# Optimization experiments

Measured on AMD Instinct MI355X. Metric: run time of the kernel, lower is better.

The kernel has to match this reference:

```python
import jax, jax.numpy as jnp
import numpy as np

B, S, D, H = 4, 1024, 1024, 16
HD = D // H  # head dim = 64


def setup_inputs() -> dict:
    key = jax.random.key(0)
    ks = jax.random.split(key, 12)
    inv = 1.0 / np.sqrt(D)
    inp = {
        "q": jax.random.normal(ks[0], (B, S, D), jnp.float32),
        "k": jax.random.normal(ks[1], (B, S, D), jnp.float32),
        "v": jax.random.normal(ks[2], (B, S, D), jnp.float32),
        # additive-style mask: 1 where attention is disallowed (causal)
        "mask": jnp.triu(jnp.ones((S, S), jnp.float32), k=1)[None, None, :, :],
        "Wq": jax.random.normal(ks[3], (D, D), jnp.float32) * inv,
        "bq": jnp.zeros((D,), jnp.float32),
        "Wk": jax.random.normal(ks[4], (D, D), jnp.float32) * inv,
        "bk": jnp.zeros((D,), jnp.float32),
        "Wv": jax.random.normal(ks[5], (D, D), jnp.float32) * inv,
        "bv": jnp.zeros((D,), jnp.float32),
        "Wo": jax.random.normal(ks[6], (D, D), jnp.float32) * inv,
        "bo": jnp.zeros((D,), jnp.float32),
    }
    return inp


def _split_heads(x):
    # [b, s, (h d)] -> [b, h, s, d]
    b, s, _ = x.shape
    return x.reshape(b, s, H, HD).transpose(0, 2, 1, 3)


def reference(q, k, v, mask, Wq, bq, Wk, bk, Wv, bv, Wo, bo):
    query = _split_heads(q @ Wq + bq)   # [b,h,s,d]
    key = _split_heads(k @ Wk + bk)
    value = _split_heads(v @ Wv + bv)

    scores = jnp.einsum("bhqd,bhkd->bhqk", query, key) / np.sqrt(HD)
    scores = scores + mask * (-1e12)
    attention_weights = jax.nn.softmax(scores, axis=-1)  # [b,h,s,s]
    attn = jnp.einsum("bhqk,bhkd->bhqd", attention_weights, value)

    # dropout is identity in eval mode
    attn = attn.transpose(0, 2, 1, 3).reshape(q.shape[0], q.shape[1], D)
    out = attn @ Wo + bo
    return out, attention_weights
```

## Files before the change

### kernel.cpp

```cpp
#include <hip/hip_runtime.h>
#include <hip/hip_bf16.h>

#define B_ 4
#define S_ 1024
#define D_ 1024
#define H_ 16
#define HD_ 64
#define M_ (B_*S_)
#define NT_ (S_/64)

typedef __attribute__((ext_vector_type(8))) short bf16x8;
typedef __attribute__((ext_vector_type(8))) unsigned short u16x8;
typedef __attribute__((ext_vector_type(4))) float f32x4;

typedef __attribute__((address_space(1))) const unsigned int g_uint;
typedef __attribute__((address_space(3))) unsigned int l_uint;

__device__ __forceinline__ unsigned short f2bf(float f) {
  unsigned int x = __builtin_bit_cast(unsigned int, f);
  unsigned int r = (x + 0x7fffu + ((x >> 16) & 1u)) >> 16;
  return (unsigned short)r;
}
__device__ __forceinline__ float bf2f(unsigned short u) {
  unsigned int x = ((unsigned int)u) << 16;
  return __builtin_bit_cast(float, x);
}
__device__ __forceinline__ unsigned int cvtpk(float lo, float hi) {
  unsigned int r;
  asm("v_cvt_pk_bf16_f32 %0, %1, %2" : "=v"(r) : "v"(lo), "v"(hi));
  return r;
}
__device__ __forceinline__ void load_lds16(const ushort* g, ushort* l) {
  __builtin_amdgcn_global_load_lds((g_uint*)g, (l_uint*)l, 16, 0, 0);
}
__device__ __forceinline__ void store_nt(float* p, f32x4 v) {
  __builtin_nontemporal_store(v, (f32x4*)p);
}

__global__ void trW(const float* __restrict__ Wq, const float* __restrict__ Wk,
                    const float* __restrict__ Wv, const float* __restrict__ Wo,
                    ushort* __restrict__ q, ushort* __restrict__ k,
                    ushort* __restrict__ v, ushort* __restrict__ o) {
  const float* W; ushort* WT;
  switch (blockIdx.z) {
    case 0: W = Wq; WT = q; break;
    case 1: W = Wk; WT = k; break;
    case 2: W = Wv; WT = v; break;
    default: W = Wo; WT = o; break;
  }
  __shared__ float tile[32][33];
  int tx = threadIdx.x & 31, ty = threadIdx.x >> 5;
  int bx = blockIdx.x * 32, by = blockIdx.y * 32;
  for (int r = 0; r < 32; r += 8)
    tile[ty + r][tx] = W[(size_t)(by + ty + r) * D_ + bx + tx];
  __syncthreads();
  for (int r = 0; r < 32; r += 8)
    WT[(size_t)(bx + ty + r) * D_ + by + tx] = f2bf(tile[tx][ty + r]);
}

template <int BF16OUT, int BM, int BN, int AFP32>
__device__ __forceinline__ void gemm_body(const void* __restrict__ Ap,
                                          const ushort* __restrict__ Bt,
                                          const float* __restrict__ bias,
                                          void* __restrict__ Cp,
                                          int bm, int bn, int N, int K) {
  __shared__ ushort Al[BM * 64];
  __shared__ ushort Bl[BN * 64];
  constexpr int MF = BM / 32;
  constexpr int NF = BN / 32;
  const int tid = threadIdx.x;
  const int wave = tid >> 6, lane = tid & 63;
  const int r0 = lane & 15, kq = lane >> 4;
  const int wr = wave >> 1, wc = wave & 1;
  const int sl = lane >> 3;
  const int sc8 = ((lane & 7) ^ sl) * 8;
  f32x4 zero = {0.f, 0.f, 0.f, 0.f};
  f32x4 acc[MF][NF];
#pragma unroll
  for (int m = 0; m < MF; ++m)
#pragma unroll
    for (int n = 0; n < NF; ++n) acc[m][n] = zero;

  for (int kt = 0; kt < K; kt += 64) {
    __syncthreads();
    if (AFP32) {
      const float* A = (const float*)Ap;
#pragma unroll
      for (int i = 0; i < MF; ++i) {
        int c = wave * MF + i;
        const float* src = &A[(size_t)(bm + c * 8 + sl) * K + kt + sc8];
        float4 f0 = *(const float4*)src;
        float4 f1 = *(const float4*)(src + 4);
        uint4 pk;
        pk.x = cvtpk(f0.x, f0.y);
        pk.y = cvtpk(f0.z, f0.w);
        pk.z = cvtpk(f1.x, f1.y);
        pk.w = cvtpk(f1.z, f1.w);
        *(uint4*)&Al[c * 512 + lane * 8] = pk;
      }
    } else {
      const ushort* A = (const ushort*)Ap;
#pragma unroll
      for (int i = 0; i < MF; ++i) {
        int c = wave * MF + i;
        load_lds16(A + (size_t)(bm + c * 8 + sl) * K + kt + sc8, &Al[c * 512]);
      }
    }
#pragma unroll
    for (int i = 0; i < NF; ++i) {
      int c = wave * NF + i;
      load_lds16(Bt + (size_t)(bn + c * 8 + sl) * K + kt + sc8, &Bl[c * 512]);
    }
    __syncthreads();
#pragma unroll
    for (int kk = 0; kk < 2; ++kk) {
      bf16x8 a[MF], b[NF];
#pragma unroll
      for (int m = 0; m < MF; ++m)
        a[m] = *(const bf16x8*)&Al[(wr * (BM / 2) + m * 16 + r0) * 64 + (((kk * 4 + kq) ^ (r0 & 7)) * 8)];
#pragma unroll
      for (int n = 0; n < NF; ++n)
        b[n] = *(const bf16x8*)&Bl[(wc * (BN / 2) + n * 16 + r0) * 64 + (((kk * 4 + kq) ^ (r0 & 7)) * 8)];
#pragma unroll
      for (int m = 0; m < MF; ++m)
#pragma unroll
        for (int n = 0; n < NF; ++n)
          acc[m][n] = __builtin_amdgcn_mfma_f32_16x16x32_bf16(a[m], b[n], acc[m][n], 0, 0, 0);
    }
  }

#pragma unroll
  for (int m = 0; m < MF; ++m) {
#pragma unroll
    for (int n = 0; n < NF; ++n) {
      int col = bn + wc * (BN / 2) + n * 16 + r0;
      float bv = bias[col];
#pragma unroll
      for (int j = 0; j < 4; ++j) {
        int row = bm + wr * (BM / 2) + m * 16 + kq * 4 + j;
        float v = acc[m][n][j] + bv;
        if (BF16OUT) ((ushort*)Cp)[(size_t)row * N + col] = f2bf(v);
        else         ((float*)Cp)[(size_t)row * N + col] = v;
      }
    }
  }
}

__global__ __launch_bounds__(256) void gemm_qkv(const float* __restrict__ qa,
                                                const float* __restrict__ ka,
                                                const float* __restrict__ va,
                                                const ushort* __restrict__ WqT,
                                                const ushort* __restrict__ WkT,
                                                const ushort* __restrict__ WvT,
                                                const float* __restrict__ bq,
                                                const float* __restrict__ bk,
                                                const float* __restrict__ bv,
                                                ushort* __restrict__ Qo,
                                                ushort* __restrict__ Ko,
                                                ushort* __restrict__ Vo) {
  const float* A; const ushort* Bt; const float* bias; ushort* C;
  switch (blockIdx.z) {
    case 0: A = qa; Bt = WqT; bias = bq; C = Qo; break;
    case 1: A = ka; Bt = WkT; bias = bk; C = Ko; break;
    default: A = va; Bt = WvT; bias = bv; C = Vo; break;
  }
  gemm_body<1, 64, 128, 1>(A, Bt, bias, C, blockIdx.x * 64, blockIdx.y * 128, D_, D_);
}

__global__ __launch_bounds__(256) void gemm_out(const ushort* __restrict__ A,
                                                const ushort* __restrict__ Bt,
                                                const float* __restrict__ bias,
                                                float* __restrict__ C) {
  gemm_body<0, 64, 64, 0>(A, Bt, bias, C, blockIdx.x * 64, blockIdx.y * 64, D_, D_);
}

__global__ __launch_bounds__(256) void attn_fused(const ushort* __restrict__ Qb,
                                                  const ushort* __restrict__ Kb,
                                                  const ushort* __restrict__ Vb,
                                                  float* __restrict__ wout,
                                                  ushort* __restrict__ ctx) {
  const int id = blockIdx.x;
  const int bh = id & 63;
  const int b = bh >> 4, h = bh & 15;
  const int p = id >> 6;
  const int qtA = NT_ - 1 - p;
  const int qtB = p;
  const int tid = threadIdx.x, wave = tid >> 6, lane = tid & 63;
  const int r0 = lane & 15, kq = lane >> 4;
  const int sl = lane >> 3;
  const int sc8 = ((lane & 7) ^ sl) * 8;
  __shared__ ushort Kt[2][64 * 64];
  __shared__ ushort Vt[2][64 * 64];
  __shared__ ushort Wl[4][16 * 64];
  const size_t bh_off = ((size_t)(b * S_)) * D_ + (size_t)h * 64;
  float* wbase = wout + (size_t)bh * S_ * S_;
  const float KSC = 0.18033688011f;

  const ushort* QgA = Qb + bh_off + (size_t)(qtA * 64 + wave * 16 + r0) * D_ + kq * 8;
  bf16x8 qa0A = *(const bf16x8*)QgA;
  bf16x8 qa1A = *(const bf16x8*)(QgA + 32);
  const ushort* QgB = Qb + bh_off + (size_t)(qtB * 64 + wave * 16 + r0) * D_ + kq * 8;
  bf16x8 qa0B = *(const bf16x8*)QgB;
  bf16x8 qa1B = *(const bf16x8*)(QgB + 32);
  const int qgA = qtA * 64 + wave * 16 + r0;
  const int qgB = qtB * 64 + wave * 16 + r0;

  auto stage_K = [&](int buf, int vb) {
    const ushort* Kg = Kb + bh_off + (size_t)(vb * 64) * D_;
#pragma unroll
    for (int i = 0; i < 2; ++i) {
      int c = wave * 2 + i;
      load_lds16(Kg + (size_t)(c * 8 + sl) * D_ + sc8, &Kt[buf][c * 512]);
    }
  };
  uint4 vr[2];
  auto vload = [&](int vb) {
    const ushort* Vg = Vb + bh_off + (size_t)(vb * 64) * D_;
    vr[0] = *(const uint4*)&Vg[(size_t)lane * D_ + (size_t)(wave * 2 + 0) * 8];
    vr[1] = *(const uint4*)&Vg[(size_t)lane * D_ + (size_t)(wave * 2 + 1) * 8];
  };
  auto vwrite = [&](int buf) {
#pragma unroll
    for (int it = 0; it < 2; ++it) {
      int seg = wave * 2 + it;
      ushort tmp[8];
      *(uint4*)tmp = vr[it];
#pragma unroll
      for (int e = 0; e < 8; ++e) Vt[buf][(seg * 8 + e) * 64 + (lane ^ (e << 3))] = tmp[e];
    }
  };

  f32x4 zero = {0.f, 0.f, 0.f, 0.f};

  int cur = 0;
  stage_K(0, 0);
  float pA0 = 0.f, pA1 = 0.f, pA2 = 0.f, pA3 = 0.f;
  for (int vb = 0; vb <= qtA; ++vb) {
    asm volatile("s_waitcnt vmcnt(0)" ::: "memory");
    __builtin_amdgcn_s_barrier();
    if (vb < qtA) stage_K(cur ^ 1, vb + 1);
    const bool diag = (vb == qtA);
#pragma unroll
    for (int jt = 0; jt < 4; ++jt) {
      int krow = jt * 16 + r0;
      bf16x8 kb0 = *(const bf16x8*)&Kt[cur][krow * 64 + ((kq ^ (r0 & 7)) * 8)];
      bf16x8 kb1 = *(const bf16x8*)&Kt[cur][krow * 64 + (((4 + kq) ^ (r0 & 7)) * 8)];
      f32x4 sc = {0.f, 0.f, 0.f, 0.f};
      sc = __builtin_amdgcn_mfma_f32_16x16x32_bf16(kb0, qa0A, sc, 0, 0, 0);
      sc = __builtin_amdgcn_mfma_f32_16x16x32_bf16(kb1, qa1A, sc, 0, 0, 0);
      int k0 = vb * 64 + jt * 16 + kq * 4;
      pA0 += (diag && k0 + 0 > qgA) ? 0.f : exp2f(sc[0] * KSC);
      pA1 += (diag && k0 + 1 > qgA) ? 0.f : exp2f(sc[1] * KSC);
      pA2 += (diag && k0 + 2 > qgA) ? 0.f : exp2f(sc[2] * KSC);
      pA3 += (diag && k0 + 3 > qgA) ? 0.f : exp2f(sc[3] * KSC);
    }
    cur ^= 1;
  }
  float ssumA = (pA0 + pA1) + (pA2 + pA3);
  ssumA += __shfl_xor(ssumA, 16, 64);
  ssumA += __shfl_xor(ssumA, 32, 64);
  const float rsA = 1.f / ssumA;

  f32x4 caccA[4];
#pragma unroll
  for (int nt = 0; nt < 4; ++nt) caccA[nt] = zero;
  float pB0 = 0.f, pB1 = 0.f, pB2 = 0.f, pB3 = 0.f;

  __syncthreads();
  cur = 0;
  stage_K(0, 0);
  vload(0);
  vwrite(0);
  for (int vb = 0; vb <= qtA; ++vb) {
    if (vb == 0) asm volatile("s_waitcnt vmcnt(0) lgkmcnt(0)" ::: "memory");
    else         asm volatile("s_waitcnt vmcnt(4) lgkmcnt(0)" ::: "memory");
    __builtin_amdgcn_s_barrier();
    if (vb < qtA) { stage_K(cur ^ 1, vb + 1); vload(vb + 1); }
    const bool diagA = (vb == qtA);
    const bool doB = (vb <= qtB);
    const bool diagB = (vb == qtB);
#pragma unroll
    for (int jt = 0; jt < 4; ++jt) {
      int krow = jt * 16 + r0;
      bf16x8 kb0 = *(const bf16x8*)&Kt[cur][krow * 64 + ((kq ^ (r0 & 7)) * 8)];
      bf16x8 kb1 = *(const bf16x8*)&Kt[cur][krow * 64 + (((4 + kq) ^ (r0 & 7)) * 8)];
      int k0 = vb * 64 + jt * 16 + kq * 4;
      f32x4 sc = {0.f, 0.f, 0.f, 0.f};
      sc = __builtin_amdgcn_mfma_f32_16x16x32_bf16(kb0, qa0A, sc, 0, 0, 0);
      sc = __builtin_amdgcn_mfma_f32_16x16x32_bf16(kb1, qa1A, sc, 0, 0, 0);
      float e0 = (diagA && k0 + 0 > qgA) ? 0.f : exp2f(sc[0] * KSC);
      float e1 = (diagA && k0 + 1 > qgA) ? 0.f : exp2f(sc[1] * KSC);
      float e2 = (diagA && k0 + 2 > qgA) ? 0.f : exp2f(sc[2] * KSC);
      float e3 = (diagA && k0 + 3 > qgA) ? 0.f : exp2f(sc[3] * KSC);
      uint2 pk;
      pk.x = cvtpk(e0, e1);
      pk.y = cvtpk(e2, e3);
      int s = (4 * jt + kq) ^ ((r0 & 3) << 2);
      *(uint2*)&Wl[wave][r0 * 64 + s * 4] = pk;
      f32x4 o = {e0 * rsA, e1 * rsA, e2 * rsA, e3 * rsA};
      store_nt(&wbase[(size_t)qgA * S_ + k0], o);
      if (doB) {
        f32x4 sb = {0.f, 0.f, 0.f, 0.f};
        sb = __builtin_amdgcn_mfma_f32_16x16x32_bf16(kb0, qa0B, sb, 0, 0, 0);
        sb = __builtin_amdgcn_mfma_f32_16x16x32_bf16(kb1, qa1B, sb, 0, 0, 0);
        pB0 += (diagB && k0 + 0 > qgB) ? 0.f : exp2f(sb[0] * KSC);
        pB1 += (diagB && k0 + 1 > qgB) ? 0.f : exp2f(sb[1] * KSC);
        pB2 += (diagB && k0 + 2 > qgB) ? 0.f : exp2f(sb[2] * KSC);
        pB3 += (diagB && k0 + 3 > qgB) ? 0.f : exp2f(sb[3] * KSC);
      }
    }
#pragma unroll
    for (int ks = 0; ks < 2; ++ks) {
      int sB = (8 * ks + 2 * kq) ^ ((r0 & 3) << 2);
      bf16x8 af = *(const bf16x8*)&Wl[wave][r0 * 64 + sB * 4];
#pragma unroll
      for (int nt = 0; nt < 4; ++nt) {
        bf16x8 vf = *(const bf16x8*)&Vt[cur][(nt * 16 + r0) * 64 + (((ks * 4 + kq) ^ (r0 & 7)) * 8)];
        caccA[nt] = __builtin_amdgcn_mfma_f32_16x16x32_bf16(af, vf, caccA[nt], 0, 0, 0);
      }
    }
    if (vb < qtA) vwrite(cur ^ 1);
    cur ^= 1;
  }
  float ssumB = (pB0 + pB1) + (pB2 + pB3);
  ssumB += __shfl_xor(ssumB, 16, 64);
  ssumB += __shfl_xor(ssumB, 32, 64);
  const float rsB = 1.f / ssumB;

  {
    int col0 = (qtA + 1) * 64;
    int nf4 = (S_ - col0) >> 2;
    int row = tid >> 2, c = tid & 3;
    f32x4 z4 = {0.f, 0.f, 0.f, 0.f};
    float* rp = &wbase[(size_t)(qtA * 64 + row) * S_];
    for (int i = c; i < nf4; i += 4) store_nt(&rp[col0 + i * 4], z4);
  }
  {
    float rsj[4];
#pragma unroll
    for (int j = 0; j < 4; ++j) rsj[j] = __shfl(rsA, kq * 4 + j, 64);
    ushort* cg = ctx + ((size_t)(b * S_ + qtA * 64 + wave * 16 + kq * 4)) * D_ + h * 64;
#pragma unroll
    for (int nt = 0; nt < 4; ++nt)
#pragma unroll
      for (int j = 0; j < 4; ++j)
        cg[(size_t)j * D_ + nt * 16 + r0] = f2bf(caccA[nt][j] * rsj[j]);
  }

  f32x4 caccB[4];
#pragma unroll
  for (int nt = 0; nt < 4; ++nt) caccB[nt] = zero;
  __syncthreads();
  cur = 0;
  stage_K(0, 0);
  vload(0);
  vwrite(0);
  for (int vb = 0; vb <= qtB; ++vb) {
    if (vb == 0) asm volatile("s_waitcnt vmcnt(0) lgkmcnt(0)" ::: "memory");
    else         asm volatile("s_waitcnt vmcnt(4) lgkmcnt(0)" ::: "memory");
    __builtin_amdgcn_s_barrier();
    if (vb < qtB) { stage_K(cur ^ 1, vb + 1); vload(vb + 1); }
    const bool diag = (vb == qtB);
#pragma unroll
    for (int jt = 0; jt < 4; ++jt) {
      int krow = jt * 16 + r0;
      bf16x8 kb0 = *(const bf16x8*)&Kt[cur][krow * 64 + ((kq ^ (r0 & 7)) * 8)];
      bf16x8 kb1 = *(const bf16x8*)&Kt[cur][krow * 64 + (((4 + kq) ^ (r0 & 7)) * 8)];
      f32x4 sc = {0.f, 0.f, 0.f, 0.f};
      sc = __builtin_amdgcn_mfma_f32_16x16x32_bf16(kb0, qa0B, sc, 0, 0, 0);
      sc = __builtin_amdgcn_mfma_f32_16x16x32_bf16(kb1, qa1B, sc, 0, 0, 0);
      int k0 = vb * 64 + jt * 16 + kq * 4;
      float e0 = (diag && k0 + 0 > qgB) ? 0.f : exp2f(sc[0] * KSC);
      float e1 = (diag && k0 + 1 > qgB) ? 0.f : exp2f(sc[1] * KSC);
      float e2 = (diag && k0 + 2 > qgB) ? 0.f : exp2f(sc[2] * KSC);
      float e3 = (diag && k0 + 3 > qgB) ? 0.f : exp2f(sc[3] * KSC);
      uint2 pk;
      pk.x = cvtpk(e0, e1);
      pk.y = cvtpk(e2, e3);
      int s = (4 * jt + kq) ^ ((r0 & 3) << 2);
      *(uint2*)&Wl[wave][r0 * 64 + s * 4] = pk;
      f32x4 o = {e0 * rsB, e1 * rsB, e2 * rsB, e3 * rsB};
      store_nt(&wbase[(size_t)qgB * S_ + k0], o);
    }
#pragma unroll
    for (int ks = 0; ks < 2; ++ks) {
      int sB = (8 * ks + 2 * kq) ^ ((r0 & 3) << 2);
      bf16x8 af = *(const bf16x8*)&Wl[wave][r0 * 64 + sB * 4];
#pragma unroll
      for (int nt = 0; nt < 4; ++nt) {
        bf16x8 vf = *(const bf16x8*)&Vt[cur][(nt * 16 + r0) * 64 + (((ks * 4 + kq) ^ (r0 & 7)) * 8)];
        caccB[nt] = __builtin_amdgcn_mfma_f32_16x16x32_bf16(af, vf, caccB[nt], 0, 0, 0);
      }
    }
    if (vb < qtB) vwrite(cur ^ 1);
    cur ^= 1;
  }

  {
    int col0 = (qtB + 1) * 64;
    int nf4 = (S_ - col0) >> 2;
    int row = tid >> 2, c = tid & 3;
    f32x4 z4 = {0.f, 0.f, 0.f, 0.f};
    float* rp = &wbase[(size_t)(qtB * 64 + row) * S_];
    for (int i = c; i < nf4; i += 4) store_nt(&rp[col0 + i * 4], z4);
  }
  {
    float rsj[4];
#pragma unroll
    for (int j = 0; j < 4; ++j) rsj[j] = __shfl(rsB, kq * 4 + j, 64);
    ushort* cg = ctx + ((size_t)(b * S_ + qtB * 64 + wave * 16 + kq * 4)) * D_ + h * 64;
#pragma unroll
    for (int nt = 0; nt < 4; ++nt)
#pragma unroll
      for (int j = 0; j < 4; ++j)
        cg[(size_t)j * D_ + nt * 16 + r0] = f2bf(caccB[nt][j] * rsj[j]);
  }
}

extern "C" void kernel_launch(void* const* d_in, const int* in_sizes, int n_in,
                              void* d_out, int out_size, void* d_ws, size_t ws_size,
                              hipStream_t stream) {
  const float* q    = (const float*)d_in[0];
  const float* k    = (const float*)d_in[1];
  const float* v    = (const float*)d_in[2];
  const float* Wq   = (const float*)d_in[4];
  const float* bq   = (const float*)d_in[5];
  const float* Wk   = (const float*)d_in[6];
  const float* bk   = (const float*)d_in[7];
  const float* Wv   = (const float*)d_in[8];
  const float* bv   = (const float*)d_in[9];
  const float* Wo   = (const float*)d_in[10];
  const float* bo   = (const float*)d_in[11];

  char* ws = (char*)d_ws;
  const size_t MB = 1024 * 1024;
  ushort* WqT    = (ushort*)(ws + 24 * MB);
  ushort* WkT    = (ushort*)(ws + 26 * MB);
  ushort* WvT    = (ushort*)(ws + 28 * MB);
  ushort* WoT    = (ushort*)(ws + 30 * MB);
  ushort* Q_bf   = (ushort*)(ws + 32 * MB);
  ushort* K_bf   = (ushort*)(ws + 40 * MB);
  ushort* V_bf   = (ushort*)(ws + 48 * MB);
  ushort* ctx_bf = (ushort*)(ws + 56 * MB);

  float* out  = (float*)d_out;
  float* wout = out + (size_t)M_ * D_;

  trW<<<dim3(32, 32, 4), 256, 0, stream>>>(Wq, Wk, Wv, Wo, WqT, WkT, WvT, WoT);
  gemm_qkv<<<dim3(M_ / 64, D_ / 128, 3), 256, 0, stream>>>(
      q, k, v, WqT, WkT, WvT, bq, bk, bv, Q_bf, K_bf, V_bf);
  attn_fused<<<dim3(512), 256, 0, stream>>>(Q_bf, K_bf, V_bf, wout, ctx_bf);
  gemm_out<<<dim3(M_ / 64, D_ / 64), 256, 0, stream>>>(ctx_bf, WoT, bo, out);
}
```

Before: 192.3 us.

## Process four query tiles per attention block sharing K/V staging passes

Each attention block now handles four query tiles (15-g, g, 8+g, 7-g) instead of two, and the grid shrinks from 512 to 256 blocks. One pass over K computes all four row sums, and a second pass over K/V computes all four weight outputs and contexts, so K/V are staged from global memory fewer times per tile. Nontemporal stores are replaced by plain vector stores, and the masked zero region is written per lane in the main tiling. The cost is higher register and LDS pressure (four accumulators and four Wl buffers), and 256 blocks may underfill the CUs on this GPU.

Result: no change. 190.2 us (-1.1%).

```diff
diff --git a/kernel.cpp b/kernel.cpp
--- a/kernel.cpp
+++ b/kernel.cpp
@@ -32,9 +32,6 @@
 }
 __device__ __forceinline__ void load_lds16(const ushort* g, ushort* l) {
   __builtin_amdgcn_global_load_lds((g_uint*)g, (l_uint*)l, 16, 0, 0);
-}
-__device__ __forceinline__ void store_nt(float* p, f32x4 v) {
-  __builtin_nontemporal_store(v, (f32x4*)p);
 }
 
 __global__ void trW(const float* __restrict__ Wq, const float* __restrict__ Wk,
@@ -182,28 +179,30 @@
   const int id = blockIdx.x;
   const int bh = id & 63;
   const int b = bh >> 4, h = bh & 15;
-  const int p = id >> 6;
-  const int qtA = NT_ - 1 - p;
-  const int qtB = p;
+  const int g = id >> 6;
+  const int qtv[4] = {15 - g, g, 8 + g, 7 - g};
+  const int max_qt = 15 - g;
   const int tid = threadIdx.x, wave = tid >> 6, lane = tid & 63;
   const int r0 = lane & 15, kq = lane >> 4;
   const int sl = lane >> 3;
   const int sc8 = ((lane & 7) ^ sl) * 8;
   __shared__ ushort Kt[2][64 * 64];
   __shared__ ushort Vt[2][64 * 64];
-  __shared__ ushort Wl[4][16 * 64];
+  __shared__ ushort Wl[4][4][16 * 64];
   const size_t bh_off = ((size_t)(b * S_)) * D_ + (size_t)h * 64;
   float* wbase = wout + (size_t)bh * S_ * S_;
   const float KSC = 0.18033688011f;
-
-  const ushort* QgA = Qb + bh_off + (size_t)(qtA * 64 + wave * 16 + r0) * D_ + kq * 8;
-  bf16x8 qa0A = *(const bf16x8*)QgA;
-  bf16x8 qa1A = *(const bf16x8*)(QgA + 32);
-  const ushort* QgB = Qb + bh_off + (size_t)(qtB * 64 + wave * 16 + r0) * D_ + kq * 8;
-  bf16x8 qa0B = *(const bf16x8*)QgB;
-  bf16x8 qa1B = *(const bf16x8*)(QgB + 32);
-  const int qgA = qtA * 64 + wave * 16 + r0;
-  const int qgB = qtB * 64 + wave * 16 + r0;
+  f32x4 zero = {0.f, 0.f, 0.f, 0.f};
+
+  bf16x8 qa0[4], qa1[4];
+  int qg[4];
+#pragma unroll
+  for (int i = 0; i < 4; ++i) {
+    const ushort* Qg = Qb + bh_off + (size_t)(qtv[i] * 64 + wave * 16 + r0) * D_ + kq * 8;
+    qa0[i] = *(const bf16x8*)Qg;
+    qa1[i] = *(const bf16x8*)(Qg + 32);
+    qg[i] = qtv[i] * 64 + wave * 16 + r0;
+  }
 
   auto stage_K = [&](int buf, int vb) {
     const ushort* Kg = Kb + bh_off + (size_t)(vb * 64) * D_;
@@ -230,190 +229,134 @@
     }
   };
 
-  f32x4 zero = {0.f, 0.f, 0.f, 0.f};
-
   int cur = 0;
   stage_K(0, 0);
-  float pA0 = 0.f, pA1 = 0.f, pA2 = 0.f, pA3 = 0.f;
-  for (int vb = 0; vb <= qtA; ++vb) {
+  float part[4][4];
+#pragma unroll
+  for (int i = 0; i < 4; ++i)
+#pragma unroll
+    for (int j = 0; j < 4; ++j) part[i][j] = 0.f;
+
+  for (int vb = 0; vb <= max_qt; ++vb) {
     asm volatile("s_waitcnt vmcnt(0)" ::: "memory");
     __builtin_amdgcn_s_barrier();
-    if (vb < qtA) stage_K(cur ^ 1, vb + 1);
-    const bool diag = (vb == qtA);
+    if (vb < max_qt) stage_K(cur ^ 1, vb + 1);
 #pragma unroll
     for (int jt = 0; jt < 4; ++jt) {
       int krow = jt * 16 + r0;
       bf16x8 kb0 = *(const bf16x8*)&Kt[cur][krow * 64 + ((kq ^ (r0 & 7)) * 8)];
       bf16x8 kb1 = *(const bf16x8*)&Kt[cur][krow * 64 + (((4 + kq) ^ (r0 & 7)) * 8)];
-      f32x4 sc = {0.f, 0.f, 0.f, 0.f};
-      sc = __builtin_amdgcn_mfma_f32_16x16x32_bf16(kb0, qa0A, sc, 0, 0, 0);
-      sc = __builtin_amdgcn_mfma_f32_16x16x32_bf16(kb1, qa1A, sc, 0, 0, 0);
       int k0 = vb * 64 + jt * 16 + kq * 4;
-      pA0 += (diag && k0 + 0 > qgA) ? 0.f : exp2f(sc[0] * KSC);
-      pA1 += (diag && k0 + 1 > qgA) ? 0.f : exp2f(sc[1] * KSC);
-      pA2 += (diag && k0 + 2 > qgA) ? 0.f : exp2f(sc[2] * KSC);
-      pA3 += (diag && k0 + 3 > qgA) ? 0.f : exp2f(sc[3] * KSC);
+#pragma unroll
+      for (int i = 0; i < 4; ++i) {
+        if (vb <= qtv[i]) {
+          f32x4 sc = {0.f, 0.f, 0.f, 0.f};
+          sc = __builtin_amdgcn_mfma_f32_16x16x32_bf16(kb0, qa0[i], sc, 0, 0, 0);
+          sc = __builtin_amdgcn_mfma_f32_16x16x32_bf16(kb1, qa1[i], sc, 0, 0, 0);
+          const bool diag = (vb == qtv[i]);
+#pragma unroll
+          for (int j = 0; j < 4; ++j)
+            part[i][j] += (diag && k0 + j > qg[i]) ? 0.f : exp2f(sc[j] * KSC);
+        }
+      }
     }
     cur ^= 1;
   }
-  float ssumA = (pA0 + pA1) + (pA2 + pA3);
-  ssumA += __shfl_xor(ssumA, 16, 64);
-  ssumA += __shfl_xor(ssumA, 32, 64);
-  const float rsA = 1.f / ssumA;
-
-  f32x4 caccA[4];
-#pragma unroll
-  for (int nt = 0; nt < 4; ++nt) caccA[nt] = zero;
-  float pB0 = 0.f, pB1 = 0.f, pB2 = 0.f, pB3 = 0.f;
+  float rs[4];
+#pragma unroll
+  for (int i = 0; i < 4; ++i) {
+    float s = (part[i][0] + part[i][1]) + (part[i][2] + part[i][3]);
+    s += __shfl_xor(s, 16, 64);
+    s += __shfl_xor(s, 32, 64);
+    rs[i] = 1.f / s;
+  }
+
+  f32x4 cacc[4][4];
+#pragma unroll
+  for (int i = 0; i < 4; ++i)
+#pragma unroll
+    for (int nt = 0; nt < 4; ++nt) cacc[i][nt] = zero;
 
   __syncthreads();
   cur = 0;
   stage_K(0, 0);
   vload(0);
   vwrite(0);
-  for (int vb = 0; vb <= qtA; ++vb) {
+  for (int vb = 0; vb <= max_qt; ++vb) {
     if (vb == 0) asm volatile("s_waitcnt vmcnt(0) lgkmcnt(0)" ::: "memory");
-    else         asm volatile("s_waitcnt vmcnt(4) lgkmcnt(0)" ::: "memory");
+    else         asm volatile("s_waitcnt vmcnt(16) lgkmcnt(0)" ::: "memory");
     __builtin_amdgcn_s_barrier();
-    if (vb < qtA) { stage_K(cur ^ 1, vb + 1); vload(vb + 1); }
-    const bool diagA = (vb == qtA);
-    const bool doB = (vb <= qtB);
-    const bool diagB = (vb == qtB);
+    if (vb < max_qt) { stage_K(cur ^ 1, vb + 1); vload(vb + 1); }
 #pragma unroll
     for (int jt = 0; jt < 4; ++jt) {
       int krow = jt * 16 + r0;
       bf16x8 kb0 = *(const bf16x8*)&Kt[cur][krow * 64 + ((kq ^ (r0 & 7)) * 8)];
       bf16x8 kb1 = *(const bf16x8*)&Kt[cur][krow * 64 + (((4 + kq) ^ (r0 & 7)) * 8)];
       int k0 = vb * 64 + jt * 16 + kq * 4;
-      f32x4 sc = {0.f, 0.f, 0.f, 0.f};
-      sc = __builtin_amdgcn_mfma_f32_16x16x32_bf16(kb0, qa0A, sc, 0, 0, 0);
-      sc = __builtin_amdgcn_mfma_f32_16x16x32_bf16(kb1, qa1A, sc, 0, 0, 0);
-      float e0 = (diagA && k0 + 0 > qgA) ? 0.f : exp2f(sc[0] * KSC);
-      float e1 = (diagA && k0 + 1 > qgA) ? 0.f : exp2f(sc[1] * KSC);
-      float e2 = (diagA && k0 + 2 > qgA) ? 0.f : exp2f(sc[2] * KSC);
-      float e3 = (diagA && k0 + 3 > qgA) ? 0.f : exp2f(sc[3] * KSC);
-      uint2 pk;
-      pk.x = cvtpk(e0, e1);
-      pk.y = cvtpk(e2, e3);
-      int s = (4 * jt + kq) ^ ((r0 & 3) << 2);
-      *(uint2*)&Wl[wave][r0 * 64 + s * 4] = pk;
-      f32x4 o = {e0 * rsA, e1 * rsA, e2 * rsA, e3 * rsA};
-      store_nt(&wbase[(size_t)qgA * S_ + k0], o);
-      if (doB) {
-        f32x4 sb = {0.f, 0.f, 0.f, 0.f};
-        sb = __builtin_amdgcn_mfma_f32_16x16x32_bf16(kb0, qa0B, sb, 0, 0, 0);
-        sb = __builtin_amdgcn_mfma_f32_16x16x32_bf16(kb1, qa1B, sb, 0, 0, 0);
-        pB0 += (diagB && k0 + 0 > qgB) ? 0.f : exp2f(sb[0] * KSC);
-        pB1 += (diagB && k0 + 1 > qgB) ? 0.f : exp2f(sb[1] * KSC);
-        pB2 += (diagB && k0 + 2 > qgB) ? 0.f : exp2f(sb[2] * KSC);
-        pB3 += (diagB && k0 + 3 > qgB) ? 0.f : exp2f(sb[3] * KSC);
-      }
-    }
-#pragma unroll
-    for (int ks = 0; ks < 2; ++ks) {
-      int sB = (8 * ks + 2 * kq) ^ ((r0 & 3) << 2);
-      bf16x8 af = *(const bf16x8*)&Wl[wave][r0 * 64 + sB * 4];
-#pragma unroll
-      for (int nt = 0; nt < 4; ++nt) {
-        bf16x8 vf = *(const bf16x8*)&Vt[cur][(nt * 16 + r0) * 64 + (((ks * 4 + kq) ^ (r0 & 7)) * 8)];
-        caccA[nt] = __builtin_amdgcn_mfma_f32_16x16x32_bf16(af, vf, caccA[nt], 0, 0, 0);
-      }
-    }
-    if (vb < qtA) vwrite(cur ^ 1);
+#pragma unroll
+      for (int i = 0; i < 4; ++i) {
+        f32x4 o;
+        if (vb <= qtv[i]) {
+          f32x4 sc = {0.f, 0.f, 0.f, 0.f};
+          sc = __builtin_amdgcn_mfma_f32_16x16x32_bf16(kb0, qa0[i], sc, 0, 0, 0);
+          sc = __builtin_amdgcn_mfma_f32_16x16x32_bf16(kb1, qa1[i], sc, 0, 0, 0);
+          const bool diag = (vb == qtv[i]);
+          float e0 = (diag && k0 + 0 > qg[i]) ? 0.f : exp2f(sc[0] * KSC);
+          float e1 = (diag && k0 + 1 > qg[i]) ? 0.f : exp2f(sc[1] * KSC);
+          float e2 = (diag && k0 + 2 > qg[i]) ? 0.f : exp2f(sc[2] * KSC);
+          float e3 = (diag && k0 + 3 > qg[i]) ? 0.f : exp2f(sc[3] * KSC);
+          uint2 pk;
+          pk.x = cvtpk(e0, e1);
+          pk.y = cvtpk(e2, e3);
+          int s = (4 * jt + kq) ^ ((r0 & 3) << 2);
+          *(uint2*)&Wl[wave][i][r0 * 64 + s * 4] = pk;
+          o[0] = e0 * rs[i]; o[1] = e1 * rs[i]; o[2] = e2 * rs[i]; o[3] = e3 * rs[i];
+        } else {
+          o = zero;
+        }
+        *(f32x4*)&wbase[(size_t)qg[i] * S_ + k0] = o;
+      }
+    }
+#pragma unroll
+    for (int i = 0; i < 4; ++i) {
+      if (vb <= qtv[i]) {
+#pragma unroll
+        for (int ks = 0; ks < 2; ++ks) {
+          int sB = (8 * ks + 2 * kq) ^ ((r0 & 3) << 2);
+          bf16x8 af = *(const bf16x8*)&Wl[wave][i][r0 * 64 + sB * 4];
+#pragma unroll
+          for (int nt = 0; nt < 4; ++nt) {
+            bf16x8 vf = *(const bf16x8*)&Vt[cur][(nt * 16 + r0) * 64 + (((ks * 4 + kq) ^ (r0 & 7)) * 8)];
+            cacc[i][nt] = __builtin_amdgcn_mfma_f32_16x16x32_bf16(af, vf, cacc[i][nt], 0, 0, 0);
+          }
+        }
+      }
+    }
+    if (vb < max_qt) vwrite(cur ^ 1);
     cur ^= 1;
   }
-  float ssumB = (pB0 + pB1) + (pB2 + pB3);
-  ssumB += __shfl_xor(ssumB, 16, 64);
-  ssumB += __shfl_xor(ssumB, 32, 64);
-  const float rsB = 1.f / ssumB;
-
-  {
-    int col0 = (qtA + 1) * 64;
-    int nf4 = (S_ - col0) >> 2;
-    int row = tid >> 2, c = tid & 3;
-    f32x4 z4 = {0.f, 0.f, 0.f, 0.f};
-    float* rp = &wbase[(size_t)(qtA * 64 + row) * S_];
-    for (int i = c; i < nf4; i += 4) store_nt(&rp[col0 + i * 4], z4);
-  }
-  {
+
+  for (int vb = max_qt + 1; vb < NT_; ++vb) {
+#pragma unroll
+    for (int jt = 0; jt < 4; ++jt) {
+      int k0 = vb * 64 + jt * 16 + kq * 4;
+#pragma unroll
+      for (int i = 0; i < 4; ++i)
+        *(f32x4*)&wbase[(size_t)qg[i] * S_ + k0] = zero;
+    }
+  }
+
+#pragma unroll
+  for (int i = 0; i < 4; ++i) {
     float rsj[4];
 #pragma unroll
-    for (int j = 0; j < 4; ++j) rsj[j] = __shfl(rsA, kq * 4 + j, 64);
-    ushort* cg = ctx + ((size_t)(b * S_ + qtA * 64 + wave * 16 + kq * 4)) * D_ + h * 64;
+    for (int j = 0; j < 4; ++j) rsj[j] = __shfl(rs[i], kq * 4 + j, 64);
+    ushort* cg = ctx + ((size_t)(b * S_ + qtv[i] * 64 + wave * 16 + kq * 4)) * D_ + h * 64;
 #pragma unroll
     for (int nt = 0; nt < 4; ++nt)
 #pragma unroll
       for (int j = 0; j < 4; ++j)
-        cg[(size_t)j * D_ + nt * 16 + r0] = f2bf(caccA[nt][j] * rsj[j]);
-  }
-
-  f32x4 caccB[4];
-#pragma unroll
-  for (int nt = 0; nt < 4; ++nt) caccB[nt] = zero;
-  __syncthreads();
-  cur = 0;
-  stage_K(0, 0);
-  vload(0);
-  vwrite(0);
-  for (int vb = 0; vb <= qtB; ++vb) {
-    if (vb == 0) asm volatile("s_waitcnt vmcnt(0) lgkmcnt(0)" ::: "memory");
-    else         asm volatile("s_waitcnt vmcnt(4) lgkmcnt(0)" ::: "memory");
-    __builtin_amdgcn_s_barrier();
-    if (vb < qtB) { stage_K(cur ^ 1, vb + 1); vload(vb + 1); }
-    const bool diag = (vb == qtB);
-#pragma unroll
-    for (int jt = 0; jt < 4; ++jt) {
-      int krow = jt * 16 + r0;
-      bf16x8 kb0 = *(const bf16x8*)&Kt[cur][krow * 64 + ((kq ^ (r0 & 7)) * 8)];
-      bf16x8 kb1 = *(const bf16x8*)&Kt[cur][krow * 64 + (((4 + kq) ^ (r0 & 7)) * 8)];
-      f32x4 sc = {0.f, 0.f, 0.f, 0.f};
-      sc = __builtin_amdgcn_mfma_f32_16x16x32_bf16(kb0, qa0B, sc, 0, 0, 0);
-      sc = __builtin_amdgcn_mfma_f32_16x16x32_bf16(kb1, qa1B, sc, 0, 0, 0);
-      int k0 = vb * 64 + jt * 16 + kq * 4;
-      float e0 = (diag && k0 + 0 > qgB) ? 0.f : exp2f(sc[0] * KSC);
-      float e1 = (diag && k0 + 1 > qgB) ? 0.f : exp2f(sc[1] * KSC);
-      float e2 = (diag && k0 + 2 > qgB) ? 0.f : exp2f(sc[2] * KSC);
-      float e3 = (diag && k0 + 3 > qgB) ? 0.f : exp2f(sc[3] * KSC);
-      uint2 pk;
-      pk.x = cvtpk(e0, e1);
-      pk.y = cvtpk(e2, e3);
-      int s = (4 * jt + kq) ^ ((r0 & 3) << 2);
-      *(uint2*)&Wl[wave][r0 * 64 + s * 4] = pk;
-      f32x4 o = {e0 * rsB, e1 * rsB, e2 * rsB, e3 * rsB};
-      store_nt(&wbase[(size_t)qgB * S_ + k0], o);
-    }
-#pragma unroll
-    for (int ks = 0; ks < 2; ++ks) {
-      int sB = (8 * ks + 2 * kq) ^ ((r0 & 3) << 2);
-      bf16x8 af = *(const bf16x8*)&Wl[wave][r0 * 64 + sB * 4];
-#pragma unroll
-      for (int nt = 0; nt < 4; ++nt) {
-        bf16x8 vf = *(const bf16x8*)&Vt[cur][(nt * 16 + r0) * 64 + (((ks * 4 + kq) ^ (r0 & 7)) * 8)];
-        caccB[nt] = __builtin_amdgcn_mfma_f32_16x16x32_bf16(af, vf, caccB[nt], 0, 0, 0);
-      }
-    }
-    if (vb < qtB) vwrite(cur ^ 1);
-    cur ^= 1;
-  }
-
-  {
-    int col0 = (qtB + 1) * 64;
-    int nf4 = (S_ - col0) >> 2;
-    int row = tid >> 2, c = tid & 3;
-    f32x4 z4 = {0.f, 0.f, 0.f, 0.f};
-    float* rp = &wbase[(size_t)(qtB * 64 + row) * S_];
-    for (int i = c; i < nf4; i += 4) store_nt(&rp[col0 + i * 4], z4);
-  }
-  {
-    float rsj[4];
-#pragma unroll
-    for (int j = 0; j < 4; ++j) rsj[j] = __shfl(rsB, kq * 4 + j, 64);
-    ushort* cg = ctx + ((size_t)(b * S_ + qtB * 64 + wave * 16 + kq * 4)) * D_ + h * 64;
-#pragma unroll
-    for (int nt = 0; nt < 4; ++nt)
-#pragma unroll
-      for (int j = 0; j < 4; ++j)
-        cg[(size_t)j * D_ + nt * 16 + r0] = f2bf(caccB[nt][j] * rsj[j]);
+        cg[(size_t)j * D_ + nt * 16 + r0] = f2bf(cacc[i][nt][j] * rsj[j]);
   }
 }
 
@@ -449,6 +392,6 @@
   trW<<<dim3(32, 32, 4), 256, 0, stream>>>(Wq, Wk, Wv, Wo, WqT, WkT, WvT, WoT);
   gemm_qkv<<<dim3(M_ / 64, D_ / 128, 3), 256, 0, stream>>>(
       q, k, v, WqT, WkT, WvT, bq, bk, bv, Q_bf, K_bf, V_bf);
-  attn_fused<<<dim3(512), 256, 0, stream>>>(Q_bf, K_bf, V_bf, wout, ctx_bf);
+  attn_fused<<<dim3(256), 256, 0, stream>>>(Q_bf, K_bf, V_bf, wout, ctx_bf);
   gemm_out<<<dim3(M_ / 64, D_ / 64), 256, 0, stream>>>(ctx_bf, WoT, bo, out);
 }
```
